# Optimization experiments

Hardware: AMD Instinct MI355X
Metric: run time of the kernel (lower is better)

## Reference

```python
import jax, jax.numpy as jnp
import numpy as np

B, S, E, H, NCTX = 32, 4095, 1024, 16, 4096  # cache len S, new seq_len = S+1
HD = E // H

def setup_inputs() -> dict:
    key = jax.random.key(0)
    ks = jax.random.split(key, 8)
    return {
        "hidden_states": jax.random.normal(ks[0], (B, 1, E), jnp.float32),
        "key_cache": jax.random.normal(ks[1], (B, S, E), jnp.float32),
        "value_cache": jax.random.normal(ks[2], (B, S, E), jnp.float32),
        "attention_mask": jnp.ones((B, S + 1), jnp.int32),
        "c_attn_w": jax.random.normal(ks[3], (E, 3 * E), jnp.float32) * 0.02,
        "c_attn_b": jax.random.normal(ks[4], (3 * E,), jnp.float32) * 0.02,
        "c_proj_w": jax.random.normal(ks[5], (E, E), jnp.float32) * 0.02,
        "c_proj_b": jax.random.normal(ks[6], (E,), jnp.float32) * 0.02,
        "attn_bias": jax.random.normal(ks[7], (NCTX, NCTX), jnp.float32) * 0.02,
    }

def reference(hidden_states, key_cache, value_cache, attention_mask,
              c_attn_w, c_attn_b, c_proj_w, c_proj_b, attn_bias):
    b, _, e = hidden_states.shape
    h, hd = H, E // H
    seq_len = key_cache.shape[1] + 1
    # fused qkv projection on the single decode token
    qkv = hidden_states[:, 0, :] @ c_attn_w + c_attn_b          # [B, 3E]
    q, k, v = jnp.split(qkv, 3, axis=-1)                         # each [B, E]
    # last valid position in attention_mask (index of last 1)
    rev = attention_mask[:, ::-1]
    last = attention_mask.shape[1] - jnp.argmax(rev, axis=1) - 1  # [B]
    # append zero column then scatter new k/v at per-batch last position
    zcol = jnp.zeros((b, 1, e), key_cache.dtype)
    bidx = jnp.arange(b)
    new_k = jnp.concatenate([key_cache, zcol], axis=1).at[bidx, last].set(k)   # [B, seq_len, E]
    new_v = jnp.concatenate([value_cache, zcol], axis=1).at[bidx, last].set(v)
    # multi-head attention with q_len = 1
    qh = q.reshape(b, h, hd)                                     # [B, H, hd]
    kh = new_k.reshape(b, seq_len, h, hd)                        # [B, S+1, H, hd]
    vh = new_v.reshape(b, seq_len, h, hd)
    scores = jnp.einsum('bhd,bshd->bhs', qh, kh) / jnp.sqrt(jnp.float32(hd))  # [B, H, S+1]
    scores = scores + attn_bias[0, :seq_len][None, None, :]
    scores = jnp.where(attention_mask[:, None, :] == 0, jnp.float32(-1e9), scores)
    w = jax.nn.softmax(scores, axis=-1)
    ctx = jnp.einsum('bhs,bshd->bhd', w, vh).reshape(b, 1, e)    # [B, 1, E]
    out = ctx @ c_proj_w + c_proj_b                               # resid_dropout is eval no-op
    return out, new_k, new_v
```

## Files before the change

kernel.cpp:

```cpp
#include <hip/hip_runtime.h>
#include <hip/hip_bf16.h>

typedef float f32x4 __attribute__((ext_vector_type(4)));

#define BATCH 32
#define S_LEN 4095
#define SEQ   4096
#define E_DIM 1024
#define NH    16
#define HD    64
#define CHUNK 64
#define NCH   (SEQ / CHUNK)

__device__ __forceinline__ f32x4 ntload4(const float* p) {
    return __builtin_nontemporal_load((const f32x4*)p);
}
__device__ __forceinline__ void ntstore4(float* p, f32x4 v) {
    __builtin_nontemporal_store(v, (f32x4*)p);
}

__global__ __launch_bounds__(256) void head_kernel(
    const int* __restrict__ mask, const float* __restrict__ bias,
    const float* __restrict__ hs, const float* __restrict__ W,
    const float* __restrict__ wb,
    int* __restrict__ lastbuf, float* __restrict__ mbias,
    float* __restrict__ qkv) {
    const int blk = blockIdx.x;
    const int t = threadIdx.x;
    if (blk < 48 * BATCH) {
        const int b = blk / 48;
        const int jblk = blk % 48;
        const int jj = t & 63;
        const int j = jblk * 64 + jj;
        const int ksl = t >> 6;
        __shared__ float h[E_DIM];
        for (int i = t; i < E_DIM; i += 256) h[i] = hs[b * E_DIM + i];
        __syncthreads();
        float acc = 0.f;
        const int k0 = ksl * 256;
        #pragma unroll 8
        for (int k = k0; k < k0 + 256; ++k) acc = fmaf(h[k], W[(size_t)k * 3072 + j], acc);
        __shared__ float red[4][64];
        red[ksl][jj] = acc;
        __syncthreads();
        if (ksl == 0)
            qkv[b * 3072 + j] = acc + red[1][jj] + red[2][jj] + red[3][jj] + wb[j];
    } else {
        const int b = blk - 48 * BATCH;
        int best = -1;
        for (int s = t; s < SEQ; s += 256) {
            int mv = mask[b * SEQ + s];
            mbias[b * SEQ + s] = mv ? bias[s] : -1.0e9f;
            if (mv) best = max(best, s);
        }
        __shared__ int red[256];
        red[t] = best;
        __syncthreads();
        for (int o = 128; o > 0; o >>= 1) {
            if (t < o) red[t] = max(red[t], red[t + o]);
            __syncthreads();
        }
        if (t == 0) lastbuf[b] = (red[0] < 0) ? (SEQ - 1) : red[0];
    }
}

__global__ __launch_bounds__(256) void attn_k_kernel(
    const float* __restrict__ kcache, const float* __restrict__ mbias,
    const float* __restrict__ qkv, const int* __restrict__ lastbuf,
    float* __restrict__ newk, float* __restrict__ wts) {
    const int c = blockIdx.x;
    const int b = blockIdx.y;
    const int t = threadIdx.x;
    const int wave = t >> 6;
    const int lane = t & 63;
    const int head = wave * 4 + (lane >> 4);
    const int lig = lane & 15;
    const int col = head * HD + lig * 4;
    const int last = lastbuf[b];

    const f32x4 q4 = *(const f32x4*)(qkv + b * 3072 + col);
    const f32x4 kn4 = *(const f32x4*)(qkv + b * 3072 + 1024 + col);
    const float* kb = kcache + (size_t)b * S_LEN * E_DIM;
    float* nkb = newk + (size_t)b * SEQ * E_DIM;
    const float* mbb = mbias + b * SEQ;

    __shared__ float sc[NH][CHUNK];
    const int s0 = c * CHUNK;
    const bool clean = (s0 + CHUNK <= S_LEN) && (last < s0 || last >= s0 + CHUNK);

    if (clean) {
        for (int r = 0; r < CHUNK; r += 8) {
            f32x4 kk[8];
            #pragma unroll
            for (int u = 0; u < 8; ++u)
                kk[u] = ntload4(kb + (size_t)(s0 + r + u) * E_DIM + col);
            #pragma unroll
            for (int u = 0; u < 8; ++u)
                ntstore4(nkb + (size_t)(s0 + r + u) * E_DIM + col, kk[u]);
            #pragma unroll
            for (int u = 0; u < 8; ++u) {
                float p = kk[u][0] * q4[0] + kk[u][1] * q4[1] + kk[u][2] * q4[2] + kk[u][3] * q4[3];
                p += __shfl_xor(p, 1);
                p += __shfl_xor(p, 2);
                p += __shfl_xor(p, 4);
                p += __shfl_xor(p, 8);
                if (lig == 0)
                    sc[head][r + u] = __expf(fmaf(p, 0.125f, mbb[s0 + r + u]));
            }
        }
    } else {
        for (int r = 0; r < CHUNK; ++r) {
            const int s = s0 + r;
            f32x4 kk;
            if (s == last) kk = kn4;
            else if (s < S_LEN) kk = ntload4(kb + (size_t)s * E_DIM + col);
            else kk = (f32x4){0.f, 0.f, 0.f, 0.f};
            ntstore4(nkb + (size_t)s * E_DIM + col, kk);
            float p = kk[0] * q4[0] + kk[1] * q4[1] + kk[2] * q4[2] + kk[3] * q4[3];
            p += __shfl_xor(p, 1);
            p += __shfl_xor(p, 2);
            p += __shfl_xor(p, 4);
            p += __shfl_xor(p, 8);
            if (lig == 0)
                sc[head][r] = __expf(fmaf(p, 0.125f, mbb[s]));
        }
    }
    __syncthreads();
    float* wblk = wts + (size_t)(b * NCH + c) * (NH * CHUNK);
    for (int idx = t; idx < NH * CHUNK; idx += 256)
        wblk[idx] = sc[idx >> 6][idx & 63];
}

__global__ __launch_bounds__(256) void attn_v_kernel(
    const float* __restrict__ vcache, const float* __restrict__ wts,
    const float* __restrict__ qkv, const int* __restrict__ lastbuf,
    float* __restrict__ newv, float* __restrict__ pl, float* __restrict__ pctx) {
    const int c = blockIdx.x;
    const int b = blockIdx.y;
    const int t = threadIdx.x;
    const int wave = t >> 6;
    const int lane = t & 63;
    const int head = wave * 4 + (lane >> 4);
    const int lig = lane & 15;
    const int col = head * HD + lig * 4;
    const int last = lastbuf[b];

    const f32x4 vn4 = *(const f32x4*)(qkv + b * 3072 + 2048 + col);
    const float* vb = vcache + (size_t)b * S_LEN * E_DIM;
    float* nvb = newv + (size_t)b * SEQ * E_DIM;

    __shared__ float w_s[NH][CHUNK];
    const float* wblk = wts + (size_t)(b * NCH + c) * (NH * CHUNK);
    for (int idx = t; idx < NH * CHUNK; idx += 256)
        w_s[idx >> 6][idx & 63] = wblk[idx];
    __syncthreads();

    float l = 0.f;
    f32x4 acc = (f32x4){0.f, 0.f, 0.f, 0.f};
    const int s0 = c * CHUNK;
    const bool clean = (s0 + CHUNK <= S_LEN) && (last < s0 || last >= s0 + CHUNK);

    if (clean) {
        for (int r = 0; r < CHUNK; r += 8) {
            f32x4 vv[8];
            #pragma unroll
            for (int u = 0; u < 8; ++u)
                vv[u] = ntload4(vb + (size_t)(s0 + r + u) * E_DIM + col);
            #pragma unroll
            for (int u = 0; u < 8; ++u)
                ntstore4(nvb + (size_t)(s0 + r + u) * E_DIM + col, vv[u]);
            #pragma unroll
            for (int u = 0; u < 8; ++u) {
                const float w = w_s[head][r + u];
                l += w;
                acc += vv[u] * w;
            }
        }
    } else {
        for (int r = 0; r < CHUNK; ++r) {
            const int s = s0 + r;
            f32x4 vv;
            if (s == last) vv = vn4;
            else if (s < S_LEN) vv = ntload4(vb + (size_t)s * E_DIM + col);
            else vv = (f32x4){0.f, 0.f, 0.f, 0.f};
            ntstore4(nvb + (size_t)s * E_DIM + col, vv);
            const float w = w_s[head][r];
            l += w;
            acc += vv * w;
        }
    }

    const int pidx = (b * NH + head) * NCH + c;
    if (lig == 0) pl[pidx] = l;
    *(f32x4*)(pctx + (size_t)pidx * HD + lig * 4) = acc;
}

__global__ __launch_bounds__(256) void reduce_kernel(const float* __restrict__ pl,
                                                     const float* __restrict__ pctx,
                                                     float* __restrict__ ctxout,
                                                     int nchunk) {
    const int gw = (blockIdx.x * blockDim.x + threadIdx.x) >> 6;
    const int lane = threadIdx.x & 63;
    if (gw >= BATCH * NH) return;
    float lacc = 0.f, cacc = 0.f;
    for (int c = 0; c < nchunk; ++c) {
        lacc += pl[gw * nchunk + c];
        cacc += pctx[(size_t)(gw * nchunk + c) * HD + lane];
    }
    ctxout[gw * HD + lane] = cacc / lacc;
}

__global__ __launch_bounds__(256) void proj_kernel(const float* __restrict__ ctx,
                                                   const float* __restrict__ W,
                                                   const float* __restrict__ bias,
                                                   float* __restrict__ out) {
    const int b = blockIdx.y;
    const int jj = threadIdx.x & 63;
    const int j = blockIdx.x * 64 + jj;
    const int ksl = threadIdx.x >> 6;
    __shared__ float h[E_DIM];
    for (int i = threadIdx.x; i < E_DIM; i += 256) h[i] = ctx[b * E_DIM + i];
    __syncthreads();
    float acc = 0.f;
    const int k0 = ksl * 256;
    #pragma unroll 8
    for (int k = k0; k < k0 + 256; ++k) acc = fmaf(h[k], W[(size_t)k * E_DIM + j], acc);
    __shared__ float red[4][64];
    red[ksl][jj] = acc;
    __syncthreads();
    if (ksl == 0)
        out[b * E_DIM + j] = acc + red[1][jj] + red[2][jj] + red[3][jj] + bias[j];
}

extern "C" void kernel_launch(void* const* d_in, const int* in_sizes, int n_in,
                              void* d_out, int out_size, void* d_ws, size_t ws_size,
                              hipStream_t stream) {
    const float* hs      = (const float*)d_in[0];
    const float* kcache  = (const float*)d_in[1];
    const float* vcache  = (const float*)d_in[2];
    const int*   mask    = (const int*)d_in[3];
    const float* attn_w  = (const float*)d_in[4];
    const float* attn_b  = (const float*)d_in[5];
    const float* proj_w  = (const float*)d_in[6];
    const float* proj_b  = (const float*)d_in[7];
    const float* bias0   = (const float*)d_in[8];

    float* out0 = (float*)d_out;
    float* newk = out0 + (size_t)BATCH * E_DIM;
    float* newv = newk + (size_t)BATCH * SEQ * E_DIM;

    float* ws = (float*)d_ws;
    float* qkv     = ws;
    float* ctxbuf  = qkv + 98304;
    float* mbias   = ctxbuf + 32768;
    float* wts     = mbias + 131072;
    float* pl      = wts + 2097152;
    float* pctx    = pl + 32768;
    int*   lastbuf = (int*)(pctx + 2097152);

    head_kernel<<<dim3(48 * BATCH + BATCH), dim3(256), 0, stream>>>(
        mask, bias0, hs, attn_w, attn_b, lastbuf, mbias, qkv);
    attn_k_kernel<<<dim3(NCH, BATCH), dim3(256), 0, stream>>>(
        kcache, mbias, qkv, lastbuf, newk, wts);
    attn_v_kernel<<<dim3(NCH, BATCH), dim3(256), 0, stream>>>(
        vcache, wts, qkv, lastbuf, newv, pl, pctx);
    reduce_kernel<<<dim3((BATCH * NH * 64 + 255) / 256), dim3(256), 0, stream>>>(
        pl, pctx, ctxbuf, NCH);
    proj_kernel<<<dim3(16, BATCH), dim3(256), 0, stream>>>(ctxbuf, proj_w, proj_b, out0);
}
```

Before: 461.5 us.

## Fuse K and V attention kernels and batch QKV/proj GEMVs across four rows

Merges the K-score and V-accumulate kernels into one, so the softmax weights stay in shared memory and are no longer written to and read back from a global workspace, and one launch goes away. The QKV and output projection kernels now handle four batch rows per block, so each weight element read from global memory is reused four times. This cuts weight traffic and block count but gives each block more work and lowers parallelism in the GEMV phases.

```diff
diff --git a/kernel.cpp b/kernel.cpp
--- a/kernel.cpp
+++ b/kernel.cpp
@@ -11,6 +11,7 @@
 #define HD    64
 #define CHUNK 64
 #define NCH   (SEQ / CHUNK)
+#define QB    4
 
 __device__ __forceinline__ f32x4 ntload4(const float* p) {
     return __builtin_nontemporal_load((const f32x4*)p);
@@ -27,26 +28,36 @@
     float* __restrict__ qkv) {
     const int blk = blockIdx.x;
     const int t = threadIdx.x;
-    if (blk < 48 * BATCH) {
-        const int b = blk / 48;
+    if (blk < 8 * 48) {
+        const int bg = blk / 48;
         const int jblk = blk % 48;
         const int jj = t & 63;
         const int j = jblk * 64 + jj;
         const int ksl = t >> 6;
-        __shared__ float h[E_DIM];
-        for (int i = t; i < E_DIM; i += 256) h[i] = hs[b * E_DIM + i];
+        __shared__ float h[QB][E_DIM];
+        for (int i = t; i < QB * E_DIM; i += 256)
+            h[i >> 10][i & 1023] = hs[(size_t)(bg * QB + (i >> 10)) * E_DIM + (i & 1023)];
         __syncthreads();
-        float acc = 0.f;
+        float acc[QB] = {0.f, 0.f, 0.f, 0.f};
         const int k0 = ksl * 256;
         #pragma unroll 8
-        for (int k = k0; k < k0 + 256; ++k) acc = fmaf(h[k], W[(size_t)k * 3072 + j], acc);
-        __shared__ float red[4][64];
-        red[ksl][jj] = acc;
+        for (int k = k0; k < k0 + 256; ++k) {
+            const float w = W[(size_t)k * 3072 + j];
+            #pragma unroll
+            for (int q = 0; q < QB; ++q) acc[q] = fmaf(h[q][k], w, acc[q]);
+        }
+        __shared__ float red[4][64][QB];
+        #pragma unroll
+        for (int q = 0; q < QB; ++q) red[ksl][jj][q] = acc[q];
         __syncthreads();
-        if (ksl == 0)
-            qkv[b * 3072 + j] = acc + red[1][jj] + red[2][jj] + red[3][jj] + wb[j];
+        if (ksl == 0) {
+            #pragma unroll
+            for (int q = 0; q < QB; ++q)
+                qkv[(size_t)(bg * QB + q) * 3072 + j] =
+                    red[0][jj][q] + red[1][jj][q] + red[2][jj][q] + red[3][jj][q] + wb[j];
+        }
     } else {
-        const int b = blk - 48 * BATCH;
+        const int b = blk - 8 * 48;
         int best = -1;
         for (int s = t; s < SEQ; s += 256) {
             int mv = mask[b * SEQ + s];
@@ -64,10 +75,12 @@
     }
 }
 
-__global__ __launch_bounds__(256) void attn_k_kernel(
-    const float* __restrict__ kcache, const float* __restrict__ mbias,
-    const float* __restrict__ qkv, const int* __restrict__ lastbuf,
-    float* __restrict__ newk, float* __restrict__ wts) {
+__global__ __launch_bounds__(256) void attn_kv_kernel(
+    const float* __restrict__ kcache, const float* __restrict__ vcache,
+    const float* __restrict__ mbias, const float* __restrict__ qkv,
+    const int* __restrict__ lastbuf,
+    float* __restrict__ newk, float* __restrict__ newv,
+    float* __restrict__ pl, float* __restrict__ pctx) {
     const int c = blockIdx.x;
     const int b = blockIdx.y;
     const int t = threadIdx.x;
@@ -78,121 +91,98 @@
     const int col = head * HD + lig * 4;
     const int last = lastbuf[b];
 
-    const f32x4 q4 = *(const f32x4*)(qkv + b * 3072 + col);
-    const f32x4 kn4 = *(const f32x4*)(qkv + b * 3072 + 1024 + col);
-    const float* kb = kcache + (size_t)b * S_LEN * E_DIM;
-    float* nkb = newk + (size_t)b * SEQ * E_DIM;
     const float* mbb = mbias + b * SEQ;
-
-    __shared__ float sc[NH][CHUNK];
+    __shared__ float w_s[NH][CHUNK];
     const int s0 = c * CHUNK;
     const bool clean = (s0 + CHUNK <= S_LEN) && (last < s0 || last >= s0 + CHUNK);
 
-    if (clean) {
-        for (int r = 0; r < CHUNK; r += 8) {
-            f32x4 kk[8];
-            #pragma unroll
-            for (int u = 0; u < 8; ++u)
-                kk[u] = ntload4(kb + (size_t)(s0 + r + u) * E_DIM + col);
-            #pragma unroll
-            for (int u = 0; u < 8; ++u)
-                ntstore4(nkb + (size_t)(s0 + r + u) * E_DIM + col, kk[u]);
-            #pragma unroll
-            for (int u = 0; u < 8; ++u) {
-                float p = kk[u][0] * q4[0] + kk[u][1] * q4[1] + kk[u][2] * q4[2] + kk[u][3] * q4[3];
+    {
+        const f32x4 q4 = *(const f32x4*)(qkv + b * 3072 + col);
+        const f32x4 kn4 = *(const f32x4*)(qkv + b * 3072 + 1024 + col);
+        const float* kb = kcache + (size_t)b * S_LEN * E_DIM;
+        float* nkb = newk + (size_t)b * SEQ * E_DIM;
+
+        if (clean) {
+            for (int r = 0; r < CHUNK; r += 8) {
+                f32x4 kk[8];
+                #pragma unroll
+                for (int u = 0; u < 8; ++u)
+                    kk[u] = ntload4(kb + (size_t)(s0 + r + u) * E_DIM + col);
+                #pragma unroll
+                for (int u = 0; u < 8; ++u)
+                    ntstore4(nkb + (size_t)(s0 + r + u) * E_DIM + col, kk[u]);
+                #pragma unroll
+                for (int u = 0; u < 8; ++u) {
+                    float p = kk[u][0] * q4[0] + kk[u][1] * q4[1] + kk[u][2] * q4[2] + kk[u][3] * q4[3];
+                    p += __shfl_xor(p, 1);
+                    p += __shfl_xor(p, 2);
+                    p += __shfl_xor(p, 4);
+                    p += __shfl_xor(p, 8);
+                    if (lig == 0)
+                        w_s[head][r + u] = __expf(fmaf(p, 0.125f, mbb[s0 + r + u]));
+                }
+            }
+        } else {
+            for (int r = 0; r < CHUNK; ++r) {
+                const int s = s0 + r;
+                f32x4 kk;
+                if (s == last) kk = kn4;
+                else if (s < S_LEN) kk = ntload4(kb + (size_t)s * E_DIM + col);
+                else kk = (f32x4){0.f, 0.f, 0.f, 0.f};
+                ntstore4(nkb + (size_t)s * E_DIM + col, kk);
+                float p = kk[0] * q4[0] + kk[1] * q4[1] + kk[2] * q4[2] + kk[3] * q4[3];
                 p += __shfl_xor(p, 1);
                 p += __shfl_xor(p, 2);
                 p += __shfl_xor(p, 4);
                 p += __shfl_xor(p, 8);
                 if (lig == 0)
-                    sc[head][r + u] = __expf(fmaf(p, 0.125f, mbb[s0 + r + u]));
-            }
-        }
-    } else {
-        for (int r = 0; r < CHUNK; ++r) {
-            const int s = s0 + r;
-            f32x4 kk;
-            if (s == last) kk = kn4;
-            else if (s < S_LEN) kk = ntload4(kb + (size_t)s * E_DIM + col);
-            else kk = (f32x4){0.f, 0.f, 0.f, 0.f};
-            ntstore4(nkb + (size_t)s * E_DIM + col, kk);
-            float p = kk[0] * q4[0] + kk[1] * q4[1] + kk[2] * q4[2] + kk[3] * q4[3];
-            p += __shfl_xor(p, 1);
-            p += __shfl_xor(p, 2);
-            p += __shfl_xor(p, 4);
-            p += __shfl_xor(p, 8);
-            if (lig == 0)
-                sc[head][r] = __expf(fmaf(p, 0.125f, mbb[s]));
+                    w_s[head][r] = __expf(fmaf(p, 0.125f, mbb[s]));
+            }
         }
     }
     __syncthreads();
-    float* wblk = wts + (size_t)(b * NCH + c) * (NH * CHUNK);
-    for (int idx = t; idx < NH * CHUNK; idx += 256)
-        wblk[idx] = sc[idx >> 6][idx & 63];
-}
-
-__global__ __launch_bounds__(256) void attn_v_kernel(
-    const float* __restrict__ vcache, const float* __restrict__ wts,
-    const float* __restrict__ qkv, const int* __restrict__ lastbuf,
-    float* __restrict__ newv, float* __restrict__ pl, float* __restrict__ pctx) {
-    const int c = blockIdx.x;
-    const int b = blockIdx.y;
-    const int t = threadIdx.x;
-    const int wave = t >> 6;
-    const int lane = t & 63;
-    const int head = wave * 4 + (lane >> 4);
-    const int lig = lane & 15;
-    const int col = head * HD + lig * 4;
-    const int last = lastbuf[b];
-
-    const f32x4 vn4 = *(const f32x4*)(qkv + b * 3072 + 2048 + col);
-    const float* vb = vcache + (size_t)b * S_LEN * E_DIM;
-    float* nvb = newv + (size_t)b * SEQ * E_DIM;
-
-    __shared__ float w_s[NH][CHUNK];
-    const float* wblk = wts + (size_t)(b * NCH + c) * (NH * CHUNK);
-    for (int idx = t; idx < NH * CHUNK; idx += 256)
-        w_s[idx >> 6][idx & 63] = wblk[idx];
-    __syncthreads();
-
-    float l = 0.f;
-    f32x4 acc = (f32x4){0.f, 0.f, 0.f, 0.f};
-    const int s0 = c * CHUNK;
-    const bool clean = (s0 + CHUNK <= S_LEN) && (last < s0 || last >= s0 + CHUNK);
-
-    if (clean) {
-        for (int r = 0; r < CHUNK; r += 8) {
-            f32x4 vv[8];
-            #pragma unroll
-            for (int u = 0; u < 8; ++u)
-                vv[u] = ntload4(vb + (size_t)(s0 + r + u) * E_DIM + col);
-            #pragma unroll
-            for (int u = 0; u < 8; ++u)
-                ntstore4(nvb + (size_t)(s0 + r + u) * E_DIM + col, vv[u]);
-            #pragma unroll
-            for (int u = 0; u < 8; ++u) {
-                const float w = w_s[head][r + u];
+
+    {
+        const f32x4 vn4 = *(const f32x4*)(qkv + b * 3072 + 2048 + col);
+        const float* vb = vcache + (size_t)b * S_LEN * E_DIM;
+        float* nvb = newv + (size_t)b * SEQ * E_DIM;
+
+        float l = 0.f;
+        f32x4 acc = (f32x4){0.f, 0.f, 0.f, 0.f};
+        if (clean) {
+            for (int r = 0; r < CHUNK; r += 8) {
+                f32x4 vv[8];
+                #pragma unroll
+                for (int u = 0; u < 8; ++u)
+                    vv[u] = ntload4(vb + (size_t)(s0 + r + u) * E_DIM + col);
+                #pragma unroll
+                for (int u = 0; u < 8; ++u)
+                    ntstore4(nvb + (size_t)(s0 + r + u) * E_DIM + col, vv[u]);
+                #pragma unroll
+                for (int u = 0; u < 8; ++u) {
+                    const float w = w_s[head][r + u];
+                    l += w;
+                    acc += vv[u] * w;
+                }
+            }
+        } else {
+            for (int r = 0; r < CHUNK; ++r) {
+                const int s = s0 + r;
+                f32x4 vv;
+                if (s == last) vv = vn4;
+                else if (s < S_LEN) vv = ntload4(vb + (size_t)s * E_DIM + col);
+                else vv = (f32x4){0.f, 0.f, 0.f, 0.f};
+                ntstore4(nvb + (size_t)s * E_DIM + col, vv);
+                const float w = w_s[head][r];
                 l += w;
-                acc += vv[u] * w;
-            }
-        }
-    } else {
-        for (int r = 0; r < CHUNK; ++r) {
-            const int s = s0 + r;
-            f32x4 vv;
-            if (s == last) vv = vn4;
-            else if (s < S_LEN) vv = ntload4(vb + (size_t)s * E_DIM + col);
-            else vv = (f32x4){0.f, 0.f, 0.f, 0.f};
-            ntstore4(nvb + (size_t)s * E_DIM + col, vv);
-            const float w = w_s[head][r];
-            l += w;
-            acc += vv * w;
-        }
-    }
-
-    const int pidx = (b * NH + head) * NCH + c;
-    if (lig == 0) pl[pidx] = l;
-    *(f32x4*)(pctx + (size_t)pidx * HD + lig * 4) = acc;
+                acc += vv * w;
+            }
+        }
+
+        const int pidx = (b * NH + head) * NCH + c;
+        if (lig == 0) pl[pidx] = l;
+        *(f32x4*)(pctx + (size_t)pidx * HD + lig * 4) = acc;
+    }
 }
 
 __global__ __launch_bounds__(256) void reduce_kernel(const float* __restrict__ pl,
@@ -214,22 +204,34 @@
                                                    const float* __restrict__ W,
                                                    const float* __restrict__ bias,
                                                    float* __restrict__ out) {
-    const int b = blockIdx.y;
-    const int jj = threadIdx.x & 63;
-    const int j = blockIdx.x * 64 + jj;
-    const int ksl = threadIdx.x >> 6;
-    __shared__ float h[E_DIM];
-    for (int i = threadIdx.x; i < E_DIM; i += 256) h[i] = ctx[b * E_DIM + i];
+    const int bg = blockIdx.y;
+    const int jblk = blockIdx.x;
+    const int t = threadIdx.x;
+    const int jj = t & 63;
+    const int j = jblk * 64 + jj;
+    const int ksl = t >> 6;
+    __shared__ float h[QB][E_DIM];
+    for (int i = t; i < QB * E_DIM; i += 256)
+        h[i >> 10][i & 1023] = ctx[(size_t)(bg * QB + (i >> 10)) * E_DIM + (i & 1023)];
     __syncthreads();
-    float acc = 0.f;
+    float acc[QB] = {0.f, 0.f, 0.f, 0.f};
     const int k0 = ksl * 256;
     #pragma unroll 8
-    for (int k = k0; k < k0 + 256; ++k) acc = fmaf(h[k], W[(size_t)k * E_DIM + j], acc);
-    __shared__ float red[4][64];
-    red[ksl][jj] = acc;
+    for (int k = k0; k < k0 + 256; ++k) {
+        const float w = W[(size_t)k * E_DIM + j];
+        #pragma unroll
+        for (int q = 0; q < QB; ++q) acc[q] = fmaf(h[q][k], w, acc[q]);
+    }
+    __shared__ float red[4][64][QB];
+    #pragma unroll
+    for (int q = 0; q < QB; ++q) red[ksl][jj][q] = acc[q];
     __syncthreads();
-    if (ksl == 0)
-        out[b * E_DIM + j] = acc + red[1][jj] + red[2][jj] + red[3][jj] + bias[j];
+    if (ksl == 0) {
+        #pragma unroll
+        for (int q = 0; q < QB; ++q)
+            out[(size_t)(bg * QB + q) * E_DIM + j] =
+                red[0][jj][q] + red[1][jj][q] + red[2][jj][q] + red[3][jj][q] + bias[j];
+    }
 }
 
 extern "C" void kernel_launch(void* const* d_in, const int* in_sizes, int n_in,
@@ -253,18 +255,15 @@
     float* qkv     = ws;
     float* ctxbuf  = qkv + 98304;
     float* mbias   = ctxbuf + 32768;
-    float* wts     = mbias + 131072;
-    float* pl      = wts + 2097152;
+    float* pl      = mbias + 131072;
     float* pctx    = pl + 32768;
     int*   lastbuf = (int*)(pctx + 2097152);
 
-    head_kernel<<<dim3(48 * BATCH + BATCH), dim3(256), 0, stream>>>(
+    head_kernel<<<dim3(8 * 48 + BATCH), dim3(256), 0, stream>>>(
         mask, bias0, hs, attn_w, attn_b, lastbuf, mbias, qkv);
-    attn_k_kernel<<<dim3(NCH, BATCH), dim3(256), 0, stream>>>(
-        kcache, mbias, qkv, lastbuf, newk, wts);
-    attn_v_kernel<<<dim3(NCH, BATCH), dim3(256), 0, stream>>>(
-        vcache, wts, qkv, lastbuf, newv, pl, pctx);
+    attn_kv_kernel<<<dim3(NCH, BATCH), dim3(256), 0, stream>>>(
+        kcache, vcache, mbias, qkv, lastbuf, newk, newv, pl, pctx);
     reduce_kernel<<<dim3((BATCH * NH * 64 + 255) / 256), dim3(256), 0, stream>>>(
         pl, pctx, ctxbuf, NCH);
-    proj_kernel<<<dim3(16, BATCH), dim3(256), 0, stream>>>(ctxbuf, proj_w, proj_b, out0);
-}
+    proj_kernel<<<dim3(16, 8), dim3(256), 0, stream>>>(ctxbuf, proj_w, proj_b, out0);
+}
```

Result: faster. 445.5 us, median of 2 (-3.5%).
